# Kernel tuning notes

Measured on AMD Instinct MI355X. Metric: run time of the kernel, lower is better.

## Reference

```python
import jax, jax.numpy as jnp
import numpy as np

N = 50000
E = 800000
IN_C, HID_C, LAT_C = 64, 64, 32


def setup_inputs() -> dict:
    key = jax.random.key(0)
    k = jax.random.split(key, 8)
    x = jax.random.normal(k[0], (N, IN_C), dtype=jnp.float32)
    edge_index = jax.random.randint(k[1], (2, E), 0, N, dtype=jnp.int64)
    edge_weight = jax.random.uniform(k[2], (E,), dtype=jnp.float32)
    # GCNConv parameters (glorot-style scale)
    W1 = jax.random.normal(k[3], (IN_C, HID_C), dtype=jnp.float32) * (1.0 / np.sqrt(IN_C))
    b1 = jnp.zeros((HID_C,), dtype=jnp.float32)
    W2 = jax.random.normal(k[4], (HID_C, LAT_C), dtype=jnp.float32) * (1.0 / np.sqrt(HID_C))
    b2 = jnp.zeros((LAT_C,), dtype=jnp.float32)
    return {"x": x, "edge_index": edge_index, "edge_weight": edge_weight,
            "W1": W1, "b1": b1, "W2": W2, "b2": b2}


def _gcn_norm(edge_index, edge_weight, num_nodes):
    # Add self loops (PyG GCNConv default: add_self_loops=True, fill_value=1.0)
    loop = jnp.arange(num_nodes, dtype=edge_index.dtype)
    src = jnp.concatenate([edge_index[0], loop])
    dst = jnp.concatenate([edge_index[1], loop])
    ew = jnp.concatenate([edge_weight, jnp.ones((num_nodes,), edge_weight.dtype)])
    # Symmetric normalization: deg computed at destination nodes
    deg = jax.ops.segment_sum(ew, dst, num_segments=num_nodes)
    dinv = jnp.where(deg > 0, jax.lax.rsqrt(deg), 0.0)
    norm = dinv[src] * ew * dinv[dst]  # [E + N]
    return src, dst, norm


def _gcn_conv(x, src, dst, norm, W, b, num_nodes):
    h = x @ W                                   # [N, out] dense transform first (out <= in)
    msg = h[src] * norm[:, None]                # gather + scale, [E+N, out]
    out = jax.ops.segment_sum(msg, dst, num_segments=num_nodes)  # scatter-add
    return out + b


def reference(x, edge_index, edge_weight, W1, b1, W2, b2):
    num_nodes = x.shape[0]
    src, dst, norm = _gcn_norm(edge_index, edge_weight, num_nodes)
    h = jax.nn.relu(_gcn_conv(x, src, dst, norm, W1, b1, num_nodes))
    z = jax.nn.relu(_gcn_conv(h, src, dst, norm, W2, b2, num_nodes))
    return z
```

## Files before the change

### kernel.cpp

```cpp
#include <hip/hip_runtime.h>
#include <hip/hip_fp16.h>

#define IN_C 64
#define HID_C 64
#define LAT_C 32
#define NMAX 50000
#define EMAX 800000
#define SLOTS 48
#define NB 196
#define CAP 5120
#define EPB 2048

__device__ float    g_dinv[NMAX];
__device__ __half   g_hf[NMAX * HID_C];
__device__ __half   g_gf[NMAX * LAT_C];
__device__ int      g_cnt[NMAX];
__device__ int      g_bcnt[NB];
__device__ uint2    g_bucket[(size_t)NB * CAP];
__device__ unsigned g_edgep[NMAX * SLOTS];


__global__ void k_zero_bcnt() {
    int i = threadIdx.x;
    if (i < NB) g_bcnt[i] = 0;
}

__global__ __launch_bounds__(256) void k_scatter1(const int* __restrict__ ei,
                                                  const float* __restrict__ ew, int E,
                                                  const float* __restrict__ x,
                                                  const float* __restrict__ W,
                                                  int n, int Bf) {
    __shared__ float sW[64 * 64];
    __shared__ float sX[4][4 * 72];
    __shared__ int hist[NB];
    __shared__ int base[NB];

    if ((int)blockIdx.x < Bf) {
        int t = threadIdx.x;
        for (int i = t; i < NB; i += 256) hist[i] = 0;
        __syncthreads();
        int e0 = blockIdx.x * EPB;
        int dv[8], sv[8], off[8];
        float wv[8];
#pragma unroll
        for (int i = 0; i < 8; ++i) {
            int e = e0 + t + i * 256;
            if (e < E) {
                dv[i] = ei[E + e];
                sv[i] = ei[e];
                wv[i] = ew[e];
                off[i] = atomicAdd(&hist[dv[i] >> 8], 1);
            } else dv[i] = -1;
        }
        __syncthreads();
        for (int i = t; i < NB; i += 256)
            base[i] = (hist[i] > 0) ? atomicAdd(&g_bcnt[i], hist[i]) : 0;
        __syncthreads();
#pragma unroll
        for (int i = 0; i < 8; ++i) {
            if (dv[i] >= 0) {
                int b = dv[i] >> 8;
                int pos = base[b] + off[i];
                if (pos < CAP) {
                    uint2 r;
                    r.x = ((unsigned)dv[i] << 16) | (unsigned)sv[i];
                    r.y = __float_as_uint(wv[i]);
                    g_bucket[(size_t)b * CAP + pos] = r;
                }
            }
        }
        return;
    }

    int bid = blockIdx.x - Bf;
    int t = threadIdx.x;
    int wave = t >> 6, lane = t & 63;
    int nodeBase = bid * 16 + wave * 4;

    {
        int w4 = lane * 4;
        int qq = w4 >> 6, kk = w4 & 63;
        int node = nodeBase + qq;
        float4 v = make_float4(0.f, 0.f, 0.f, 0.f);
        if (node < n) v = *(const float4*)&x[(size_t)node * 64 + kk];
        *(float4*)&sX[wave][qq * 72 + kk] = v;
    }
    for (int i = t * 4; i < 64 * 64; i += 256 * 4)
        *(float4*)&sW[i] = *(const float4*)&W[i];
    __syncthreads();

    int q = lane >> 4, r = lane & 15;
    float4 acc = make_float4(0.f, 0.f, 0.f, 0.f);
#pragma unroll
    for (int k4 = 0; k4 < 16; ++k4) {
        float4 xk = *(const float4*)&sX[wave][q * 72 + k4 * 4];
        float4 w0 = *(const float4*)&sW[(k4 * 4 + 0) * 64 + r * 4];
        float4 w1 = *(const float4*)&sW[(k4 * 4 + 1) * 64 + r * 4];
        float4 w2 = *(const float4*)&sW[(k4 * 4 + 2) * 64 + r * 4];
        float4 w3 = *(const float4*)&sW[(k4 * 4 + 3) * 64 + r * 4];
        acc.x += xk.x * w0.x; acc.y += xk.x * w0.y; acc.z += xk.x * w0.z; acc.w += xk.x * w0.w;
        acc.x += xk.y * w1.x; acc.y += xk.y * w1.y; acc.z += xk.y * w1.z; acc.w += xk.y * w1.w;
        acc.x += xk.z * w2.x; acc.y += xk.z * w2.y; acc.z += xk.z * w2.z; acc.w += xk.z * w2.w;
        acc.x += xk.w * w3.x; acc.y += xk.w * w3.y; acc.z += xk.w * w3.z; acc.w += xk.w * w3.w;
    }
    int node = nodeBase + q;
    if (node < n) {
        ushort4 hv;
        hv.x = __half_as_ushort(__float2half_rn(acc.x));
        hv.y = __half_as_ushort(__float2half_rn(acc.y));
        hv.z = __half_as_ushort(__float2half_rn(acc.z));
        hv.w = __half_as_ushort(__float2half_rn(acc.w));
        *(ushort4*)&g_hf[(size_t)node * 64 + r * 4] = hv;
    }
}

__global__ __launch_bounds__(256) void k_build2(int n) {
    __shared__ int   cntl[256];
    __shared__ float degl[256];
    __shared__ float dinvl[256];
    int t = threadIdx.x;
    cntl[t] = 0;
    degl[t] = 0.f;
    __syncthreads();
    int b = blockIdx.x;
    int m = min(g_bcnt[b], CAP);
    const uint2* buck = &g_bucket[(size_t)b * CAP];
    for (int i = t; i < m; i += 256) {
        uint2 r = buck[i];
        int d = r.x >> 16;
        int dloc = d & 255;
        float w = __uint_as_float(r.y);
        int slot = atomicAdd(&cntl[dloc], 1);
        atomicAdd(&degl[dloc], w);
        if (slot < SLOTS) {
            unsigned rec = ((r.x & 0xffffu) << 16) |
                           (unsigned)__half_as_ushort(__float2half_rn(w));
            g_edgep[(size_t)d * SLOTS + slot] = rec;
        }
    }
    __syncthreads();
    int d = (b << 8) + t;
    if (d < n) {
        int c = min(cntl[t], SLOTS);
        int cp8 = min((c + 7) & ~7, SLOTS);
        for (int s = c; s < cp8; ++s) g_edgep[(size_t)d * SLOTS + s] = 0;
        g_cnt[d] = min((c + 3) & ~3, SLOTS);
        float di = rsqrtf(1.0f + degl[t]);
        g_dinv[d] = di;
        dinvl[t] = di;
    }
    __syncthreads();
    int rowsBase = b << 8;
    for (int i = t; i < 256 * 32; i += 256) {
        int r = i >> 5, el = i & 31;
        int d2 = rowsBase + r;
        if (d2 < n) {
            __half2* p = (__half2*)&g_hf[(size_t)d2 * 64] + el;
            float2 v = __half22float2(*p);
            float sc = dinvl[r];
            *p = __floats2half2_rn(v.x * sc, v.y * sc);
        }
    }
}

__global__ __launch_bounds__(256) void k_gather_fuse(const float* __restrict__ b1,
                                                     const float* __restrict__ W2, int n) {
    __shared__ float sW[64 * 32];
    __shared__ float sB[64];
    __shared__ float sA[16][68];
    int t = threadIdx.x;
    for (int i = t * 4; i < 64 * 32; i += 256 * 4)
        *(float4*)&sW[i] = *(const float4*)&W2[i];
    if (t < 64) sB[t] = b1[t];

    int lane = t & 63;
    int q = lane >> 4;
    int v = lane & 15;
    int nl = (t >> 6) * 4 + q;
    int w = blockIdx.x * 16 + nl;

    int len = (w < n) ? g_cnt[w] : 0;
    int len8 = len & ~7;
    int m1 = max(len8, __shfl_xor(len8, 16, 64));
    int lenmax8 = max(m1, __shfl_xor(m1, 32, 64));
    float dd = (w < n) ? g_dinv[w] : 0.f;
    unsigned v8 = (unsigned)(v * 8);
    const char* hb = (const char*)g_hf;

    float4 a0 = make_float4(0.f, 0.f, 0.f, 0.f), a1 = a0, a2 = a0, a3 = a0;
    float4 a4 = a0, a5 = a0, a6 = a0, a7 = a0;
    if (w < n) {
        uint2 rr = *(const uint2*)(hb + ((unsigned)w << 7) + v8);
        float2 f0 = __half22float2(*(__half2*)&rr.x);
        float2 f1 = __half22float2(*(__half2*)&rr.y);
        a0.x = f0.x; a0.y = f0.y; a0.z = f1.x; a0.w = f1.y;
    }
    const unsigned* row = &g_edgep[(size_t)w * SLOTS];
#define GSTEP(ACC, E) { \
    float nn = __half2float(__ushort_as_half((unsigned short)((E) & 0xffffu))); \
    unsigned off = (((E) >> 9) & 0xFFFFFF80u) | v8; \
    uint2 rr = *(const uint2*)(hb + off); \
    float2 f0 = __half22float2(*(__half2*)&rr.x); \
    float2 f1 = __half22float2(*(__half2*)&rr.y); \
    ACC.x += f0.x * nn; ACC.y += f0.y * nn; ACC.z += f1.x * nn; ACC.w += f1.y * nn; }
    for (int j = 0; j < lenmax8; j += 8) {
        if (j < len8) {
            uint4 ra = *(const uint4*)&row[j];
            uint4 rb = *(const uint4*)&row[j + 4];
            GSTEP(a0, ra.x) GSTEP(a1, ra.y) GSTEP(a2, ra.z) GSTEP(a3, ra.w)
            GSTEP(a4, rb.x) GSTEP(a5, rb.y) GSTEP(a6, rb.z) GSTEP(a7, rb.w)
        }
    }
    if (len & 4) {
        uint4 rt = *(const uint4*)&row[len8];
        GSTEP(a0, rt.x) GSTEP(a1, rt.y) GSTEP(a2, rt.z) GSTEP(a3, rt.w)
    }
#undef GSTEP
    float4 av;
    av.x = (((a0.x + a1.x) + (a2.x + a3.x)) + ((a4.x + a5.x) + (a6.x + a7.x))) * dd;
    av.y = (((a0.y + a1.y) + (a2.y + a3.y)) + ((a4.y + a5.y) + (a6.y + a7.y))) * dd;
    av.z = (((a0.z + a1.z) + (a2.z + a3.z)) + ((a4.z + a5.z) + (a6.z + a7.z))) * dd;
    av.w = (((a0.w + a1.w) + (a2.w + a3.w)) + ((a4.w + a5.w) + (a6.w + a7.w))) * dd;
    *(float4*)&sA[nl][4 * v] = av;
    __syncthreads();

    int nl2 = t >> 4;
    int cp = t & 15;
    int w2 = blockIdx.x * 16 + nl2;
    float g0 = 0.f, g1 = 0.f;
#pragma unroll
    for (int k = 0; k < 64; k += 2) {
        float2 ap = *(const float2*)&sA[nl2][k];
        float2 bp = *(const float2*)&sB[k];
        float ak0 = fmaxf(ap.x + bp.x, 0.f);
        float ak1 = fmaxf(ap.y + bp.y, 0.f);
        float2 w0 = *(const float2*)&sW[k * 32 + 2 * cp];
        float2 w1 = *(const float2*)&sW[(k + 1) * 32 + 2 * cp];
        g0 += ak0 * w0.x + ak1 * w1.x;
        g1 += ak0 * w0.y + ak1 * w1.y;
    }
    if (w2 < n) {
        float dd2 = g_dinv[w2];
        *(__half2*)&g_gf[(size_t)w2 * 32 + 2 * cp] = __floats2half2_rn(g0 * dd2, g1 * dd2);
    }
}

__global__ __launch_bounds__(256) void k_gather32(float* __restrict__ out,
                                                  const float* __restrict__ b2, int n) {
    int t = threadIdx.x;
    int hw = (blockIdx.x * 256 + t) >> 5;
    int lane = t & 31;
    int q = lane >> 4;
    int u = lane & 15;
    if (hw >= n) return;
    int len = g_cnt[hw];
    int len8 = len & ~7;
    float dd = g_dinv[hw];
    unsigned u4 = (unsigned)(u * 4);
    const char* gb = (const char*)g_gf;
    float2 accA = make_float2(0.f, 0.f), accB = accA, accC = accA, accD = accA;
    {
        float2 sv = __half22float2(*(const __half2*)&g_gf[(size_t)hw * 32 + 2 * u]);
        float hs = q ? 0.f : 1.f;
        accA.x = sv.x * hs; accA.y = sv.y * hs;
    }
    const unsigned* row = &g_edgep[(size_t)hw * SLOTS];
#define GSTEP32(ACC, E) { \
    float nn = __half2float(__ushort_as_half((unsigned short)((E) & 0xffffu))); \
    unsigned off = (((E) >> 10) & 0xFFFFFFC0u) | u4; \
    float2 ff = __half22float2(*(const __half2*)(gb + off)); \
    ACC.x += ff.x * nn; ACC.y += ff.y * nn; }
    int j = 0;
    for (; j < len8; j += 8) {
        uint4 ra = *(const uint4*)&row[j];
        uint4 rb = *(const uint4*)&row[j + 4];
        unsigned eA = q ? ra.y : ra.x;
        unsigned eB = q ? ra.w : ra.z;
        unsigned eC = q ? rb.y : rb.x;
        unsigned eD = q ? rb.w : rb.z;
        GSTEP32(accA, eA) GSTEP32(accB, eB) GSTEP32(accC, eC) GSTEP32(accD, eD)
    }
    if (len & 4) {
        uint4 ra = *(const uint4*)&row[len8];
        unsigned eA = q ? ra.y : ra.x;
        unsigned eB = q ? ra.w : ra.z;
        GSTEP32(accA, eA) GSTEP32(accB, eB)
    }
#undef GSTEP32
    float ax = (accA.x + accB.x) + (accC.x + accD.x);
    float ay = (accA.y + accB.y) + (accC.y + accD.y);
    ax += __shfl_xor(ax, 16, 64);
    ay += __shfl_xor(ay, 16, 64);
    if (q == 0) {
        float2 o;
        o.x = fmaxf(ax * dd + b2[2 * u], 0.f);
        o.y = fmaxf(ay * dd + b2[2 * u + 1], 0.f);
        *(float2*)&out[(size_t)hw * 32 + 2 * u] = o;
    }
}


extern "C" void kernel_launch(void* const* d_in, const int* in_sizes, int n_in,
                              void* d_out, int out_size, void* d_ws, size_t ws_size,
                              hipStream_t stream) {
    const float* x  = (const float*)d_in[0];
    const int*   ei = (const int*)d_in[1];
    const float* ew = (const float*)d_in[2];
    const float* W1 = (const float*)d_in[3];
    const float* b1 = (const float*)d_in[4];
    const float* W2 = (const float*)d_in[5];
    const float* b2 = (const float*)d_in[6];
    float* out = (float*)d_out;

    int n = in_sizes[0] / IN_C;
    if (n > NMAX) n = NMAX;
    int E = in_sizes[2];
    if (E > EMAX) E = EMAX;

    int Bf = (E + EPB - 1) / EPB;
    int Bg = (n + 15) / 16;

    k_zero_bcnt<<<1, 256, 0, stream>>>();

    k_scatter1<<<Bf + Bg, 256, 0, stream>>>(ei, ew, E, x, W1, n, Bf);

    k_build2<<<NB, 256, 0, stream>>>(n);

    k_gather_fuse<<<(n + 15) / 16, 256, 0, stream>>>(b1, W2, n);

    k_gather32<<<(n * 32 + 255) / 256, 256, 0, stream>>>(out, b2, n);
}
```

Before: 96.71 us.

## Remap gather kernels to 8 lanes per node with wider 16-byte loads

Both gather kernels now assign 8 lanes per destination node instead of 16 (layer 1) or 32 (layer 2). Each lane loads 16 bytes (layer 1) or 8 bytes (layer 2) of fp16 features per edge, so one wave covers 8 nodes. Edge lists are padded only to multiples of 4, which removes the 8-edge main loop, its tail handling, the cross-lane length max, and the layer-2 shuffle reduction. The fused dense transform is reshaped to produce 4 outputs per thread over 32 nodes per block. Fewer lanes per node means more edges processed serially per lane and more register use for accumulators, in exchange for fewer, wider memory requests and less wasted padding work.

```diff
diff --git a/kernel.cpp b/kernel.cpp
--- a/kernel.cpp
+++ b/kernel.cpp
@@ -142,9 +142,9 @@
     int d = (b << 8) + t;
     if (d < n) {
         int c = min(cntl[t], SLOTS);
-        int cp8 = min((c + 7) & ~7, SLOTS);
-        for (int s = c; s < cp8; ++s) g_edgep[(size_t)d * SLOTS + s] = 0;
-        g_cnt[d] = min((c + 3) & ~3, SLOTS);
+        int cp = min((c + 3) & ~3, SLOTS);
+        for (int s = c; s < cp; ++s) g_edgep[(size_t)d * SLOTS + s] = 0;
+        g_cnt[d] = cp;
         float di = rsqrtf(1.0f + degl[t]);
         g_dinv[d] = di;
         dinvl[t] = di;
@@ -167,136 +167,124 @@
                                                      const float* __restrict__ W2, int n) {
     __shared__ float sW[64 * 32];
     __shared__ float sB[64];
-    __shared__ float sA[16][68];
+    __shared__ float sA[32][68];
     int t = threadIdx.x;
     for (int i = t * 4; i < 64 * 32; i += 256 * 4)
         *(float4*)&sW[i] = *(const float4*)&W2[i];
     if (t < 64) sB[t] = b1[t];
 
     int lane = t & 63;
-    int q = lane >> 4;
-    int v = lane & 15;
-    int nl = (t >> 6) * 4 + q;
-    int w = blockIdx.x * 16 + nl;
+    int g = lane >> 3;
+    int o = lane & 7;
+    int nl = (t >> 6) * 8 + g;
+    int w = blockIdx.x * 32 + nl;
 
     int len = (w < n) ? g_cnt[w] : 0;
-    int len8 = len & ~7;
-    int m1 = max(len8, __shfl_xor(len8, 16, 64));
-    int lenmax8 = max(m1, __shfl_xor(m1, 32, 64));
     float dd = (w < n) ? g_dinv[w] : 0.f;
-    unsigned v8 = (unsigned)(v * 8);
+    unsigned o16 = (unsigned)(o * 16);
     const char* hb = (const char*)g_hf;
 
-    float4 a0 = make_float4(0.f, 0.f, 0.f, 0.f), a1 = a0, a2 = a0, a3 = a0;
-    float4 a4 = a0, a5 = a0, a6 = a0, a7 = a0;
+    float4 s0a = make_float4(0.f, 0.f, 0.f, 0.f), s0b = s0a;
+    float4 s1a = s0a, s1b = s0a, s2a = s0a, s2b = s0a, s3a = s0a, s3b = s0a;
     if (w < n) {
-        uint2 rr = *(const uint2*)(hb + ((unsigned)w << 7) + v8);
+        uint4 rr = *(const uint4*)(hb + ((unsigned)w << 7) + o16);
         float2 f0 = __half22float2(*(__half2*)&rr.x);
         float2 f1 = __half22float2(*(__half2*)&rr.y);
-        a0.x = f0.x; a0.y = f0.y; a0.z = f1.x; a0.w = f1.y;
+        float2 f2 = __half22float2(*(__half2*)&rr.z);
+        float2 f3 = __half22float2(*(__half2*)&rr.w);
+        s0a = make_float4(f0.x, f0.y, f1.x, f1.y);
+        s0b = make_float4(f2.x, f2.y, f3.x, f3.y);
     }
     const unsigned* row = &g_edgep[(size_t)w * SLOTS];
-#define GSTEP(ACC, E) { \
+#define GSTEP8(AL, AH, E) { \
     float nn = __half2float(__ushort_as_half((unsigned short)((E) & 0xffffu))); \
-    unsigned off = (((E) >> 9) & 0xFFFFFF80u) | v8; \
-    uint2 rr = *(const uint2*)(hb + off); \
+    unsigned off = (((E) >> 9) & 0xFFFFFF80u) | o16; \
+    uint4 rr = *(const uint4*)(hb + off); \
+    float2 f0 = __half22float2(*(__half2*)&rr.x); \
+    float2 f1 = __half22float2(*(__half2*)&rr.y); \
+    float2 f2 = __half22float2(*(__half2*)&rr.z); \
+    float2 f3 = __half22float2(*(__half2*)&rr.w); \
+    AL.x += f0.x * nn; AL.y += f0.y * nn; AL.z += f1.x * nn; AL.w += f1.y * nn; \
+    AH.x += f2.x * nn; AH.y += f2.y * nn; AH.z += f3.x * nn; AH.w += f3.y * nn; }
+    for (int j = 0; j < len; j += 4) {
+        uint4 ra = *(const uint4*)&row[j];
+        GSTEP8(s0a, s0b, ra.x) GSTEP8(s1a, s1b, ra.y)
+        GSTEP8(s2a, s2b, ra.z) GSTEP8(s3a, s3b, ra.w)
+    }
+#undef GSTEP8
+    float4 avl, avh;
+    avl.x = ((s0a.x + s1a.x) + (s2a.x + s3a.x)) * dd;
+    avl.y = ((s0a.y + s1a.y) + (s2a.y + s3a.y)) * dd;
+    avl.z = ((s0a.z + s1a.z) + (s2a.z + s3a.z)) * dd;
+    avl.w = ((s0a.w + s1a.w) + (s2a.w + s3a.w)) * dd;
+    avh.x = ((s0b.x + s1b.x) + (s2b.x + s3b.x)) * dd;
+    avh.y = ((s0b.y + s1b.y) + (s2b.y + s3b.y)) * dd;
+    avh.z = ((s0b.z + s1b.z) + (s2b.z + s3b.z)) * dd;
+    avh.w = ((s0b.w + s1b.w) + (s2b.w + s3b.w)) * dd;
+    *(float4*)&sA[nl][8 * o] = avl;
+    *(float4*)&sA[nl][8 * o + 4] = avh;
+    __syncthreads();
+
+    int nl2 = t >> 3;
+    int c4 = (t & 7) * 4;
+    int w2 = blockIdx.x * 32 + nl2;
+    float4 gacc = make_float4(0.f, 0.f, 0.f, 0.f);
+#pragma unroll
+    for (int k = 0; k < 64; ++k) {
+        float ak = fmaxf(sA[nl2][k] + sB[k], 0.f);
+        float4 wk = *(const float4*)&sW[k * 32 + c4];
+        gacc.x += ak * wk.x; gacc.y += ak * wk.y;
+        gacc.z += ak * wk.z; gacc.w += ak * wk.w;
+    }
+    if (w2 < n) {
+        float dd2 = g_dinv[w2];
+        __half2 h0 = __floats2half2_rn(gacc.x * dd2, gacc.y * dd2);
+        __half2 h1 = __floats2half2_rn(gacc.z * dd2, gacc.w * dd2);
+        uint2 pk; pk.x = *(unsigned*)&h0; pk.y = *(unsigned*)&h1;
+        *(uint2*)&g_gf[(size_t)w2 * 32 + c4] = pk;
+    }
+}
+
+__global__ __launch_bounds__(256) void k_gather32(float* __restrict__ out,
+                                                  const float* __restrict__ b2, int n) {
+    int t = threadIdx.x;
+    int lane = t & 63;
+    int g = lane >> 3;
+    int v = lane & 7;
+    int hw = blockIdx.x * 32 + (t >> 6) * 8 + g;
+    if (hw >= n) return;
+    int len = g_cnt[hw];
+    float dd = g_dinv[hw];
+    unsigned v8 = (unsigned)(v * 8);
+    const char* gb = (const char*)g_gf;
+
+    float4 a0, a1 = make_float4(0.f, 0.f, 0.f, 0.f), a2 = a1, a3 = a1;
+    {
+        uint2 rr = *(const uint2*)(gb + ((unsigned)hw << 6) + v8);
+        float2 f0 = __half22float2(*(__half2*)&rr.x);
+        float2 f1 = __half22float2(*(__half2*)&rr.y);
+        a0 = make_float4(f0.x, f0.y, f1.x, f1.y);
+    }
+    const unsigned* row = &g_edgep[(size_t)hw * SLOTS];
+#define GSTEP32Q(ACC, E) { \
+    float nn = __half2float(__ushort_as_half((unsigned short)((E) & 0xffffu))); \
+    unsigned off = (((E) >> 10) & 0xFFFFFFC0u) | v8; \
+    uint2 rr = *(const uint2*)(gb + off); \
     float2 f0 = __half22float2(*(__half2*)&rr.x); \
     float2 f1 = __half22float2(*(__half2*)&rr.y); \
     ACC.x += f0.x * nn; ACC.y += f0.y * nn; ACC.z += f1.x * nn; ACC.w += f1.y * nn; }
-    for (int j = 0; j < lenmax8; j += 8) {
-        if (j < len8) {
-            uint4 ra = *(const uint4*)&row[j];
-            uint4 rb = *(const uint4*)&row[j + 4];
-            GSTEP(a0, ra.x) GSTEP(a1, ra.y) GSTEP(a2, ra.z) GSTEP(a3, ra.w)
-            GSTEP(a4, rb.x) GSTEP(a5, rb.y) GSTEP(a6, rb.z) GSTEP(a7, rb.w)
-        }
-    }
-    if (len & 4) {
-        uint4 rt = *(const uint4*)&row[len8];
-        GSTEP(a0, rt.x) GSTEP(a1, rt.y) GSTEP(a2, rt.z) GSTEP(a3, rt.w)
-    }
-#undef GSTEP
-    float4 av;
-    av.x = (((a0.x + a1.x) + (a2.x + a3.x)) + ((a4.x + a5.x) + (a6.x + a7.x))) * dd;
-    av.y = (((a0.y + a1.y) + (a2.y + a3.y)) + ((a4.y + a5.y) + (a6.y + a7.y))) * dd;
-    av.z = (((a0.z + a1.z) + (a2.z + a3.z)) + ((a4.z + a5.z) + (a6.z + a7.z))) * dd;
-    av.w = (((a0.w + a1.w) + (a2.w + a3.w)) + ((a4.w + a5.w) + (a6.w + a7.w))) * dd;
-    *(float4*)&sA[nl][4 * v] = av;
-    __syncthreads();
-
-    int nl2 = t >> 4;
-    int cp = t & 15;
-    int w2 = blockIdx.x * 16 + nl2;
-    float g0 = 0.f, g1 = 0.f;
-#pragma unroll
-    for (int k = 0; k < 64; k += 2) {
-        float2 ap = *(const float2*)&sA[nl2][k];
-        float2 bp = *(const float2*)&sB[k];
-        float ak0 = fmaxf(ap.x + bp.x, 0.f);
-        float ak1 = fmaxf(ap.y + bp.y, 0.f);
-        float2 w0 = *(const float2*)&sW[k * 32 + 2 * cp];
-        float2 w1 = *(const float2*)&sW[(k + 1) * 32 + 2 * cp];
-        g0 += ak0 * w0.x + ak1 * w1.x;
-        g1 += ak0 * w0.y + ak1 * w1.y;
-    }
-    if (w2 < n) {
-        float dd2 = g_dinv[w2];
-        *(__half2*)&g_gf[(size_t)w2 * 32 + 2 * cp] = __floats2half2_rn(g0 * dd2, g1 * dd2);
-    }
-}
-
-__global__ __launch_bounds__(256) void k_gather32(float* __restrict__ out,
-                                                  const float* __restrict__ b2, int n) {
-    int t = threadIdx.x;
-    int hw = (blockIdx.x * 256 + t) >> 5;
-    int lane = t & 31;
-    int q = lane >> 4;
-    int u = lane & 15;
-    if (hw >= n) return;
-    int len = g_cnt[hw];
-    int len8 = len & ~7;
-    float dd = g_dinv[hw];
-    unsigned u4 = (unsigned)(u * 4);
-    const char* gb = (const char*)g_gf;
-    float2 accA = make_float2(0.f, 0.f), accB = accA, accC = accA, accD = accA;
-    {
-        float2 sv = __half22float2(*(const __half2*)&g_gf[(size_t)hw * 32 + 2 * u]);
-        float hs = q ? 0.f : 1.f;
-        accA.x = sv.x * hs; accA.y = sv.y * hs;
-    }
-    const unsigned* row = &g_edgep[(size_t)hw * SLOTS];
-#define GSTEP32(ACC, E) { \
-    float nn = __half2float(__ushort_as_half((unsigned short)((E) & 0xffffu))); \
-    unsigned off = (((E) >> 10) & 0xFFFFFFC0u) | u4; \
-    float2 ff = __half22float2(*(const __half2*)(gb + off)); \
-    ACC.x += ff.x * nn; ACC.y += ff.y * nn; }
-    int j = 0;
-    for (; j < len8; j += 8) {
+    for (int j = 0; j < len; j += 4) {
         uint4 ra = *(const uint4*)&row[j];
-        uint4 rb = *(const uint4*)&row[j + 4];
-        unsigned eA = q ? ra.y : ra.x;
-        unsigned eB = q ? ra.w : ra.z;
-        unsigned eC = q ? rb.y : rb.x;
-        unsigned eD = q ? rb.w : rb.z;
-        GSTEP32(accA, eA) GSTEP32(accB, eB) GSTEP32(accC, eC) GSTEP32(accD, eD)
-    }
-    if (len & 4) {
-        uint4 ra = *(const uint4*)&row[len8];
-        unsigned eA = q ? ra.y : ra.x;
-        unsigned eB = q ? ra.w : ra.z;
-        GSTEP32(accA, eA) GSTEP32(accB, eB)
-    }
-#undef GSTEP32
-    float ax = (accA.x + accB.x) + (accC.x + accD.x);
-    float ay = (accA.y + accB.y) + (accC.y + accD.y);
-    ax += __shfl_xor(ax, 16, 64);
-    ay += __shfl_xor(ay, 16, 64);
-    if (q == 0) {
-        float2 o;
-        o.x = fmaxf(ax * dd + b2[2 * u], 0.f);
-        o.y = fmaxf(ay * dd + b2[2 * u + 1], 0.f);
-        *(float2*)&out[(size_t)hw * 32 + 2 * u] = o;
-    }
+        GSTEP32Q(a0, ra.x) GSTEP32Q(a1, ra.y) GSTEP32Q(a2, ra.z) GSTEP32Q(a3, ra.w)
+    }
+#undef GSTEP32Q
+    float4 bb = *(const float4*)&b2[4 * v];
+    float4 o4;
+    o4.x = fmaxf(((a0.x + a1.x) + (a2.x + a3.x)) * dd + bb.x, 0.f);
+    o4.y = fmaxf(((a0.y + a1.y) + (a2.y + a3.y)) * dd + bb.y, 0.f);
+    o4.z = fmaxf(((a0.z + a1.z) + (a2.z + a3.z)) * dd + bb.z, 0.f);
+    o4.w = fmaxf(((a0.w + a1.w) + (a2.w + a3.w)) * dd + bb.w, 0.f);
+    *(float4*)&out[(size_t)hw * 32 + 4 * v] = o4;
 }
 
 
@@ -326,7 +314,7 @@
 
     k_build2<<<NB, 256, 0, stream>>>(n);
 
-    k_gather_fuse<<<(n + 15) / 16, 256, 0, stream>>>(b1, W2, n);
-
-    k_gather32<<<(n * 32 + 255) / 256, 256, 0, stream>>>(out, b2, n);
-}
+    k_gather_fuse<<<(n + 31) / 32, 256, 0, stream>>>(b1, W2, n);
+
+    k_gather32<<<(n + 31) / 32, 256, 0, stream>>>(out, b2, n);
+}
```

New measurement: 93.44 us. 3.4% less time.
